# Kernel optimization log

Measured on AMD Instinct MI355X. Metric: run time of the kernel, lower is better.

The kernel has to match this reference:

```python
import jax, jax.numpy as jnp
import numpy as np

N_HEADS = 16

def setup_inputs() -> dict:
    key = jax.random.key(0)
    qkv = jax.random.normal(key, (4, 3072, 1024), dtype=jnp.float32)
    return {"qkv": qkv}

def reference(qkv):
    bs, width, length = qkv.shape
    ch = width // (3 * N_HEADS)
    qkv_h = qkv.reshape(bs * N_HEADS, 3 * ch, length)
    q, k, v = jnp.split(qkv_h, 3, axis=1)  # each [bs*H, ch, T]
    scale = 1.0 / jnp.sqrt(jnp.sqrt(jnp.asarray(ch, qkv.dtype)))
    # [bs*H, T, T] scores
    weight = jnp.einsum('bct,bcs->bts', q * scale, k * scale)
    weight = jax.nn.softmax(weight.astype(jnp.float32), axis=-1).astype(weight.dtype)
    a = jnp.einsum('bts,bcs->bct', weight, v)  # [bs*H, ch, T]
    return a.reshape(bs, -1, length)
```

## Files before the change

kernel.cpp:

```cpp
#include <hip/hip_runtime.h>
#include <hip/hip_bf16.h>


typedef __bf16 bf16_8 __attribute__((ext_vector_type(8)));
typedef __bf16 bf16_4 __attribute__((ext_vector_type(4)));
typedef float floatx4 __attribute__((ext_vector_type(4)));

#define NTHREADS 256
#define STRIDE 72
#define NSTEPS 16

#if __has_builtin(__builtin_amdgcn_exp2f)
#define EXP2(x) __builtin_amdgcn_exp2f(x)
#else
#define EXP2(x) exp2f(x)
#endif
#define QSCALE 0.18033688011112042f

#define LDS_BYTES 55296

__global__ __launch_bounds__(NTHREADS, 2)
void attn_kernel(const float* __restrict__ qkv, float* __restrict__ out) {
    __shared__ char smem[LDS_BYTES];
    __bf16* q_s = (__bf16*)smem;
    __bf16* k_s = (__bf16*)(smem + 36864);
    __bf16* v_s = (__bf16*)(smem + 46080);

    const int tid  = threadIdx.x;
    const int wave = tid >> 6;
    const int lane = tid & 63;
    const int quad = lane >> 4;
    const int i16  = lane & 15;

    const int bx = blockIdx.x;
    const int bh = bx & 63;
    const int t0 = (bx >> 6) << 8;

    const float* qg = qkv + (size_t)bh * 196608;
    const float* kg = qg + 65536;
    const float* vg = qg + 131072;

    const int si = tid & 15;
    const int sG = tid >> 4;
    const int c0 = sG << 2;

    #pragma unroll
    for (int tj = 0; tj < 4; ++tj) {
        float4 q4[4];
        #pragma unroll
        for (int jj = 0; jj < 4; ++jj)
            q4[jj] = *(const float4*)(qg + (c0 + jj) * 1024 + t0 + tj * 64 + si * 4);
        #pragma unroll
        for (int rr = 0; rr < 4; ++rr) {
            int trow = tj * 64 + si * 4 + rr;
            bf16_4 w;
            w[0] = (__bf16)(((const float*)&q4[0])[rr] * QSCALE);
            w[1] = (__bf16)(((const float*)&q4[1])[rr] * QSCALE);
            w[2] = (__bf16)(((const float*)&q4[2])[rr] * QSCALE);
            w[3] = (__bf16)(((const float*)&q4[3])[rr] * QSCALE);
            *(bf16_4*)&q_s[trow * STRIDE + ((sG ^ (trow & 14)) << 2)] = w;
        }
    }
    {
        float4 k4[4], v4[4];
        #pragma unroll
        for (int jj = 0; jj < 4; ++jj) {
            k4[jj] = *(const float4*)(kg + (c0 + jj) * 1024 + si * 4);
            v4[jj] = *(const float4*)(vg + (c0 + jj) * 1024 + si * 4);
        }
        #pragma unroll
        for (int rr = 0; rr < 4; ++rr) {
            int srow = si * 4 + rr;
            bf16_4 w;
            w[0] = (__bf16)((const float*)&k4[0])[rr];
            w[1] = (__bf16)((const float*)&k4[1])[rr];
            w[2] = (__bf16)((const float*)&k4[2])[rr];
            w[3] = (__bf16)((const float*)&k4[3])[rr];
            *(bf16_4*)&k_s[srow * STRIDE + ((sG ^ (srow & 14)) << 2)] = w;
        }
        #pragma unroll
        for (int jj = 0; jj < 4; ++jj) {
            bf16_4 w;
            w[0] = (__bf16)v4[jj].x; w[1] = (__bf16)v4[jj].y;
            w[2] = (__bf16)v4[jj].z; w[3] = (__bf16)v4[jj].w;
            *(bf16_4*)&v_s[(c0 + jj) * STRIDE + si * 4] = w;
        }
    }
    __syncthreads();

    bf16_8 qf[4][2];
    #pragma unroll
    for (int tt = 0; tt < 4; ++tt) {
        int row = wave * 64 + tt * 16 + i16;
        int e2 = (row >> 1) & 7;
        #pragma unroll
        for (int kk = 0; kk < 2; ++kk)
            qf[tt][kk] = *(const bf16_8*)&q_s[row * STRIDE + (((kk * 4 + quad) ^ e2) << 3)];
    }

    floatx4 O[4][4];
    #pragma unroll
    for (int tt = 0; tt < 4; ++tt)
        #pragma unroll
        for (int cn = 0; cn < 4; ++cn) O[tt][cn] = (floatx4){0.f, 0.f, 0.f, 0.f};
    float l[4] = {0.f, 0.f, 0.f, 0.f};

    __bf16* pw = q_s + (size_t)(wave * 64) * STRIDE;

    for (int is = 0; is < NSTEPS; ++is) {
        float4 kr[4], vr[4];
        if (is < NSTEPS - 1) {
            const int s0n = (is + 1) * 64;
            #pragma unroll
            for (int jj = 0; jj < 4; ++jj) {
                kr[jj] = *(const float4*)(kg + (c0 + jj) * 1024 + s0n + si * 4);
                vr[jj] = *(const float4*)(vg + (c0 + jj) * 1024 + s0n + si * 4);
            }
        }

        floatx4 St[4][4];
        #pragma unroll
        for (int sb = 0; sb < 4; ++sb) {
            int srow = sb * 16 + i16;
            int e2 = (srow >> 1) & 7;
            bf16_8 kf0 = *(const bf16_8*)&k_s[srow * STRIDE + ((quad ^ e2) << 3)];
            bf16_8 kf1 = *(const bf16_8*)&k_s[srow * STRIDE + (((4 + quad) ^ e2) << 3)];
            #pragma unroll
            for (int tt = 0; tt < 4; ++tt) {
                floatx4 acc = __builtin_amdgcn_mfma_f32_16x16x32_bf16(
                    kf0, qf[tt][0], (floatx4){0.f, 0.f, 0.f, 0.f}, 0, 0, 0);
                St[tt][sb] = __builtin_amdgcn_mfma_f32_16x16x32_bf16(
                    kf1, qf[tt][1], acc, 0, 0, 0);
            }
        }
        #pragma unroll
        for (int tt = 0; tt < 4; ++tt)
            #pragma unroll
            for (int sb = 0; sb < 4; ++sb) {
                float p0 = EXP2(St[tt][sb][0]);
                float p1 = EXP2(St[tt][sb][1]);
                float p2 = EXP2(St[tt][sb][2]);
                float p3 = EXP2(St[tt][sb][3]);
                l[tt] += (p0 + p1) + (p2 + p3);
                bf16_4 pk;
                pk[0] = (__bf16)p0; pk[1] = (__bf16)p1;
                pk[2] = (__bf16)p2; pk[3] = (__bf16)p3;
                *(bf16_4*)&pw[(tt * 16 + i16) * STRIDE + sb * 16 + quad * 4] = pk;
            }
        bf16_8 af[4][2];
        #pragma unroll
        for (int tt = 0; tt < 4; ++tt)
            #pragma unroll
            for (int kk = 0; kk < 2; ++kk)
                af[tt][kk] = *(const bf16_8*)&pw[(tt * 16 + i16) * STRIDE + kk * 32 + quad * 8];
        #pragma unroll
        for (int cn = 0; cn < 4; ++cn)
            #pragma unroll
            for (int kk = 0; kk < 2; ++kk) {
                bf16_8 vf = *(const bf16_8*)&v_s[(cn * 16 + i16) * STRIDE + kk * 32 + quad * 8];
                #pragma unroll
                for (int tt = 0; tt < 4; ++tt)
                    O[tt][cn] = __builtin_amdgcn_mfma_f32_16x16x32_bf16(
                        vf, af[tt][kk], O[tt][cn], 0, 0, 0);
            }

        if (is < NSTEPS - 1) {
            __syncthreads();
            #pragma unroll
            for (int rr = 0; rr < 4; ++rr) {
                int srow = si * 4 + rr;
                bf16_4 w;
                w[0] = (__bf16)((const float*)&kr[0])[rr];
                w[1] = (__bf16)((const float*)&kr[1])[rr];
                w[2] = (__bf16)((const float*)&kr[2])[rr];
                w[3] = (__bf16)((const float*)&kr[3])[rr];
                *(bf16_4*)&k_s[srow * STRIDE + ((sG ^ (srow & 14)) << 2)] = w;
            }
            #pragma unroll
            for (int jj = 0; jj < 4; ++jj) {
                bf16_4 w;
                w[0] = (__bf16)vr[jj].x; w[1] = (__bf16)vr[jj].y;
                w[2] = (__bf16)vr[jj].z; w[3] = (__bf16)vr[jj].w;
                *(bf16_4*)&v_s[(c0 + jj) * STRIDE + si * 4] = w;
            }
            __syncthreads();
        }
    }

    float* og = out + (size_t)bh * 65536 + t0 + wave * 64;
    #pragma unroll
    for (int tt = 0; tt < 4; ++tt) {
        float s = l[tt];
        s += __shfl_xor(s, 16);
        s += __shfl_xor(s, 32);
        const float linv = 1.0f / s;
        #pragma unroll
        for (int cn = 0; cn < 4; ++cn)
            #pragma unroll
            for (int r = 0; r < 4; ++r)
                og[(cn * 16 + 4 * quad + r) * 1024 + tt * 16 + i16] = O[tt][cn][r] * linv;
    }
}

extern "C" void kernel_launch(void* const* d_in, const int* in_sizes, int n_in,
                              void* d_out, int out_size, void* d_ws, size_t ws_size,
                              hipStream_t stream) {
    const float* qkv = (const float*)d_in[0];
    float* out = (float*)d_out;
    attn_kernel<<<dim3(256), dim3(NTHREADS), 0, stream>>>(qkv, out);
}
```

Baseline: 114.9 us.

## Halve query tile per block, double-buffer K/V in LDS, new XOR swizzle

Each block now handles 128 query rows instead of 256, doubling the grid to 512 blocks so more CUs are busy (256 blocks underfill the device). K and V tiles are double-buffered in LDS, which cuts the two barriers per step down to one, and the padded stride is replaced by an unpadded 64-element stride with an XOR swizzle to avoid bank conflicts. The trade-off is that K/V are reloaded from global memory twice as often and each wave gets less MFMA work per K/V load.

```diff
diff --git a/kernel.cpp b/kernel.cpp
--- a/kernel.cpp
+++ b/kernel.cpp
@@ -7,7 +7,7 @@
 typedef float floatx4 __attribute__((ext_vector_type(4)));
 
 #define NTHREADS 256
-#define STRIDE 72
+#define STR 64
 #define NSTEPS 16
 
 #if __has_builtin(__builtin_amdgcn_exp2f)
@@ -17,14 +17,18 @@
 #endif
 #define QSCALE 0.18033688011112042f
 
-#define LDS_BYTES 55296
+#define LDS_BYTES 49152
+
+__device__ __forceinline__ int kap(int row) { return ((row >> 1) + (row >> 4)) & 7; }
 
 __global__ __launch_bounds__(NTHREADS, 2)
 void attn_kernel(const float* __restrict__ qkv, float* __restrict__ out) {
     __shared__ char smem[LDS_BYTES];
     __bf16* q_s = (__bf16*)smem;
-    __bf16* k_s = (__bf16*)(smem + 36864);
-    __bf16* v_s = (__bf16*)(smem + 46080);
+    __bf16* k0  = (__bf16*)(smem + 16384);
+    __bf16* k1  = (__bf16*)(smem + 24576);
+    __bf16* v0  = (__bf16*)(smem + 32768);
+    __bf16* v1  = (__bf16*)(smem + 40960);
 
     const int tid  = threadIdx.x;
     const int wave = tid >> 6;
@@ -34,7 +38,7 @@
 
     const int bx = blockIdx.x;
     const int bh = bx & 63;
-    const int t0 = (bx >> 6) << 8;
+    const int t0 = (bx >> 6) << 7;
 
     const float* qg = qkv + (size_t)bh * 196608;
     const float* kg = qg + 65536;
@@ -45,20 +49,23 @@
     const int c0 = sG << 2;
 
     #pragma unroll
-    for (int tj = 0; tj < 4; ++tj) {
+    for (int j = 0; j < 2; ++j) {
+        int f  = j * NTHREADS + tid;
+        int cG = f >> 5;
+        int ti = f & 31;
         float4 q4[4];
         #pragma unroll
         for (int jj = 0; jj < 4; ++jj)
-            q4[jj] = *(const float4*)(qg + (c0 + jj) * 1024 + t0 + tj * 64 + si * 4);
+            q4[jj] = *(const float4*)(qg + (cG * 4 + jj) * 1024 + t0 + ti * 4);
         #pragma unroll
         for (int rr = 0; rr < 4; ++rr) {
-            int trow = tj * 64 + si * 4 + rr;
+            int trow = ti * 4 + rr;
             bf16_4 w;
             w[0] = (__bf16)(((const float*)&q4[0])[rr] * QSCALE);
             w[1] = (__bf16)(((const float*)&q4[1])[rr] * QSCALE);
             w[2] = (__bf16)(((const float*)&q4[2])[rr] * QSCALE);
             w[3] = (__bf16)(((const float*)&q4[3])[rr] * QSCALE);
-            *(bf16_4*)&q_s[trow * STRIDE + ((sG ^ (trow & 14)) << 2)] = w;
+            *(bf16_4*)&q_s[trow * STR + ((cG ^ (kap(trow) << 1)) << 2)] = w;
         }
     }
     {
@@ -76,38 +83,44 @@
             w[1] = (__bf16)((const float*)&k4[1])[rr];
             w[2] = (__bf16)((const float*)&k4[2])[rr];
             w[3] = (__bf16)((const float*)&k4[3])[rr];
-            *(bf16_4*)&k_s[srow * STRIDE + ((sG ^ (srow & 14)) << 2)] = w;
+            *(bf16_4*)&k0[srow * STR + ((sG ^ (kap(srow) << 1)) << 2)] = w;
         }
         #pragma unroll
         for (int jj = 0; jj < 4; ++jj) {
+            int c = c0 + jj;
             bf16_4 w;
             w[0] = (__bf16)v4[jj].x; w[1] = (__bf16)v4[jj].y;
             w[2] = (__bf16)v4[jj].z; w[3] = (__bf16)v4[jj].w;
-            *(bf16_4*)&v_s[(c0 + jj) * STRIDE + si * 4] = w;
+            *(bf16_4*)&v0[c * STR + ((si ^ (kap(c) << 1)) << 2)] = w;
         }
     }
     __syncthreads();
 
-    bf16_8 qf[4][2];
-    #pragma unroll
-    for (int tt = 0; tt < 4; ++tt) {
-        int row = wave * 64 + tt * 16 + i16;
-        int e2 = (row >> 1) & 7;
+    bf16_8 qf[2][2];
+    #pragma unroll
+    for (int tt = 0; tt < 2; ++tt) {
+        int row = wave * 32 + tt * 16 + i16;
+        int x = kap(row);
         #pragma unroll
         for (int kk = 0; kk < 2; ++kk)
-            qf[tt][kk] = *(const bf16_8*)&q_s[row * STRIDE + (((kk * 4 + quad) ^ e2) << 3)];
-    }
-
-    floatx4 O[4][4];
-    #pragma unroll
-    for (int tt = 0; tt < 4; ++tt)
+            qf[tt][kk] = *(const bf16_8*)&q_s[row * STR + ((((kk << 2) | quad) ^ x) << 3)];
+    }
+
+    floatx4 O[2][4];
+    #pragma unroll
+    for (int tt = 0; tt < 2; ++tt)
         #pragma unroll
         for (int cn = 0; cn < 4; ++cn) O[tt][cn] = (floatx4){0.f, 0.f, 0.f, 0.f};
-    float l[4] = {0.f, 0.f, 0.f, 0.f};
-
-    __bf16* pw = q_s + (size_t)(wave * 64) * STRIDE;
+    float l[2] = {0.f, 0.f};
+
+    __bf16* pw = q_s + (size_t)(wave * 32) * STR;
+    const int xp0 = (i16 >> 1) & 7;
+    const int xv  = 0;
 
     for (int is = 0; is < NSTEPS; ++is) {
+        const __bf16* kc = (is & 1) ? k1 : k0;
+        const __bf16* vc = (is & 1) ? v1 : v0;
+
         float4 kr[4], vr[4];
         if (is < NSTEPS - 1) {
             const int s0n = (is + 1) * 64;
@@ -118,23 +131,26 @@
             }
         }
 
-        floatx4 St[4][4];
+        floatx4 St[2][4];
         #pragma unroll
         for (int sb = 0; sb < 4; ++sb) {
             int srow = sb * 16 + i16;
-            int e2 = (srow >> 1) & 7;
-            bf16_8 kf0 = *(const bf16_8*)&k_s[srow * STRIDE + ((quad ^ e2) << 3)];
-            bf16_8 kf1 = *(const bf16_8*)&k_s[srow * STRIDE + (((4 + quad) ^ e2) << 3)];
-            #pragma unroll
-            for (int tt = 0; tt < 4; ++tt) {
-                floatx4 acc = __builtin_amdgcn_mfma_f32_16x16x32_bf16(
-                    kf0, qf[tt][0], (floatx4){0.f, 0.f, 0.f, 0.f}, 0, 0, 0);
-                St[tt][sb] = __builtin_amdgcn_mfma_f32_16x16x32_bf16(
-                    kf1, qf[tt][1], acc, 0, 0, 0);
-            }
-        }
-        #pragma unroll
-        for (int tt = 0; tt < 4; ++tt)
+            int x = (sb + (i16 >> 1)) & 7;
+            bf16_8 kf0 = *(const bf16_8*)&kc[srow * STR + ((quad ^ x) << 3)];
+            bf16_8 kf1 = *(const bf16_8*)&kc[srow * STR + (((4 | quad) ^ x) << 3)];
+            floatx4 a0 = (floatx4){0.f, 0.f, 0.f, 0.f};
+            floatx4 a1 = (floatx4){0.f, 0.f, 0.f, 0.f};
+            a0 = __builtin_amdgcn_mfma_f32_16x16x32_bf16(kf0, qf[0][0], a0, 0, 0, 0);
+            a0 = __builtin_amdgcn_mfma_f32_16x16x32_bf16(kf1, qf[0][1], a0, 0, 0, 0);
+            a1 = __builtin_amdgcn_mfma_f32_16x16x32_bf16(kf0, qf[1][0], a1, 0, 0, 0);
+            a1 = __builtin_amdgcn_mfma_f32_16x16x32_bf16(kf1, qf[1][1], a1, 0, 0, 0);
+            St[0][sb] = a0;
+            St[1][sb] = a1;
+        }
+        #pragma unroll
+        for (int tt = 0; tt < 2; ++tt) {
+            int trow = tt * 16 + i16;
+            int xp = (tt + xp0) & 7;
             #pragma unroll
             for (int sb = 0; sb < 4; ++sb) {
                 float p0 = EXP2(St[tt][sb][0]);
@@ -145,27 +161,34 @@
                 bf16_4 pk;
                 pk[0] = (__bf16)p0; pk[1] = (__bf16)p1;
                 pk[2] = (__bf16)p2; pk[3] = (__bf16)p3;
-                *(bf16_4*)&pw[(tt * 16 + i16) * STRIDE + sb * 16 + quad * 4] = pk;
-            }
-        bf16_8 af[4][2];
-        #pragma unroll
-        for (int tt = 0; tt < 4; ++tt)
+                int ch = ((sb << 2) | quad) ^ (xp << 1);
+                *(bf16_4*)&pw[trow * STR + (ch << 2)] = pk;
+            }
+        }
+        bf16_8 af[2][2];
+        #pragma unroll
+        for (int tt = 0; tt < 2; ++tt) {
+            int trow = tt * 16 + i16;
+            int xp = (tt + xp0) & 7;
             #pragma unroll
             for (int kk = 0; kk < 2; ++kk)
-                af[tt][kk] = *(const bf16_8*)&pw[(tt * 16 + i16) * STRIDE + kk * 32 + quad * 8];
-        #pragma unroll
-        for (int cn = 0; cn < 4; ++cn)
+                af[tt][kk] = *(const bf16_8*)&pw[trow * STR + ((((kk << 2) | quad) ^ xp) << 3)];
+        }
+        #pragma unroll
+        for (int cn = 0; cn < 4; ++cn) {
+            int crow = cn * 16 + i16;
+            int xc = (cn + (i16 >> 1)) & 7;
             #pragma unroll
             for (int kk = 0; kk < 2; ++kk) {
-                bf16_8 vf = *(const bf16_8*)&v_s[(cn * 16 + i16) * STRIDE + kk * 32 + quad * 8];
-                #pragma unroll
-                for (int tt = 0; tt < 4; ++tt)
-                    O[tt][cn] = __builtin_amdgcn_mfma_f32_16x16x32_bf16(
-                        vf, af[tt][kk], O[tt][cn], 0, 0, 0);
-            }
+                bf16_8 vf = *(const bf16_8*)&vc[crow * STR + ((((kk << 2) | quad) ^ xc) << 3)];
+                O[0][cn] = __builtin_amdgcn_mfma_f32_16x16x32_bf16(vf, af[0][kk], O[0][cn], 0, 0, 0);
+                O[1][cn] = __builtin_amdgcn_mfma_f32_16x16x32_bf16(vf, af[1][kk], O[1][cn], 0, 0, 0);
+            }
+        }
 
         if (is < NSTEPS - 1) {
-            __syncthreads();
+            __bf16* kn = (is & 1) ? k0 : k1;
+            __bf16* vn = (is & 1) ? v0 : v1;
             #pragma unroll
             for (int rr = 0; rr < 4; ++rr) {
                 int srow = si * 4 + rr;
@@ -174,22 +197,23 @@
                 w[1] = (__bf16)((const float*)&kr[1])[rr];
                 w[2] = (__bf16)((const float*)&kr[2])[rr];
                 w[3] = (__bf16)((const float*)&kr[3])[rr];
-                *(bf16_4*)&k_s[srow * STRIDE + ((sG ^ (srow & 14)) << 2)] = w;
+                *(bf16_4*)&kn[srow * STR + ((sG ^ (kap(srow) << 1)) << 2)] = w;
             }
             #pragma unroll
             for (int jj = 0; jj < 4; ++jj) {
+                int c = c0 + jj;
                 bf16_4 w;
                 w[0] = (__bf16)vr[jj].x; w[1] = (__bf16)vr[jj].y;
                 w[2] = (__bf16)vr[jj].z; w[3] = (__bf16)vr[jj].w;
-                *(bf16_4*)&v_s[(c0 + jj) * STRIDE + si * 4] = w;
-            }
-            __syncthreads();
-        }
-    }
-
-    float* og = out + (size_t)bh * 65536 + t0 + wave * 64;
-    #pragma unroll
-    for (int tt = 0; tt < 4; ++tt) {
+                *(bf16_4*)&vn[c * STR + ((si ^ (kap(c) << 1)) << 2)] = w;
+            }
+        }
+        __syncthreads();
+    }
+
+    float* og = out + (size_t)bh * 65536 + t0 + wave * 32;
+    #pragma unroll
+    for (int tt = 0; tt < 2; ++tt) {
         float s = l[tt];
         s += __shfl_xor(s, 16);
         s += __shfl_xor(s, 32);
@@ -207,5 +231,5 @@
                               hipStream_t stream) {
     const float* qkv = (const float*)d_in[0];
     float* out = (float*)d_out;
-    attn_kernel<<<dim3(256), dim3(NTHREADS), 0, stream>>>(qkv, out);
+    attn_kernel<<<dim3(512), dim3(NTHREADS), 0, stream>>>(qkv, out);
 }
```

Measured after the change: 106.3 us. 7.5% less time.
